# Kernel tuning notes

Measured on AMD Instinct MI355X. Metric: run time of the kernel, lower is better.

## Reference

```python
import jax, jax.numpy as jnp
import numpy as np

WH, WW = 12, 12          # window height/width
N = WH * WW              # tokens per window (144)
HEADS = 16
DIM = 1024
C = DIM // 2             # attention channel dim (512)
HEAD_DIM = C // HEADS    # 32


def _rel_pos_index(wh, ww):
    ch, cw = np.arange(wh), np.arange(ww)
    coords = np.stack(np.meshgrid(ch, cw, indexing='ij')).reshape(2, -1)  # [2, N]
    rel = (coords[:, :, None] - coords[:, None, :]).transpose(1, 2, 0)    # [N, N, 2]
    rel = rel.copy()
    rel[:, :, 0] += wh - 1
    rel[:, :, 1] += ww - 1
    rel[:, :, 0] *= 2 * ww - 1
    return rel.sum(-1)  # [N, N] int


def _layernorm(x, g, b, eps=1e-5):
    mu = jnp.mean(x, axis=-1, keepdims=True)
    var = jnp.mean(jnp.square(x - mu), axis=-1, keepdims=True)
    return (x - mu) * jax.lax.rsqrt(var + eps) * g + b


def setup_inputs():
    key = jax.random.key(0)
    ks = jax.random.split(key, 10)
    std = 0.02
    inp = {
        'x': jax.random.normal(ks[0], (256, N, DIM), jnp.float32),
        'template': jax.random.normal(ks[1], (64, N, DIM), jnp.float32),
        'mask0': jnp.zeros((16, N, N), jnp.float32),
        'mask1': jnp.zeros((4, N, N), jnp.float32),
        's_H': 48, 's_W': 48, 't_H': 24, 't_W': 24,
        'rpb_table': jax.random.normal(ks[2], ((2 * WH - 1) * (2 * WW - 1), HEADS), jnp.float32) * std,
        'w_ps': jax.random.normal(ks[3], (DIM, C), jnp.float32) * std,
        'b_ps': jnp.zeros((C,), jnp.float32),
        'g_ps': jnp.ones((C,), jnp.float32),
        'be_ps': jnp.zeros((C,), jnp.float32),
        'w_pt': jax.random.normal(ks[4], (DIM, C), jnp.float32) * std,
        'b_pt': jnp.zeros((C,), jnp.float32),
        'g_pt': jnp.ones((C,), jnp.float32),
        'be_pt': jnp.zeros((C,), jnp.float32),
        'w_qkv': jax.random.normal(ks[5], (C, 3 * C), jnp.float32) * std,
        'b_qkv': jnp.zeros((3 * C,), jnp.float32),
        'w_tr': jax.random.normal(ks[6], (C, DIM), jnp.float32) * std,
        'b_tr': jnp.zeros((DIM,), jnp.float32),
        'w_sr': jax.random.normal(ks[7], (C, DIM), jnp.float32) * std,
        'b_sr': jnp.zeros((DIM,), jnp.float32),
    }
    return inp


def reference(x, template, mask0, mask1, s_H, s_W, t_H, t_W,
              rpb_table, w_ps, b_ps, g_ps, be_ps, w_pt, b_pt, g_pt, be_pt,
              w_qkv, b_qkv, w_tr, b_tr, w_sr, b_sr):
    scale = HEAD_DIM ** (-0.5)
    search_attn = _layernorm(x @ w_ps + b_ps, g_ps, be_ps)          # [Sw, N, C]
    template_attn = _layernorm(template @ w_pt + b_pt, g_pt, be_pt)  # [Tw, N, C]
    Sw, Tw = search_attn.shape[0], template_attn.shape[0]
    xa = jnp.concatenate([template_attn, search_attn], axis=0)      # [B_, N, C]
    B_, n, c = xa.shape

    qkv = (xa @ w_qkv + b_qkv).reshape(B_, n, 3, HEADS, HEAD_DIM)
    q = qkv[:, :, 0].transpose(0, 2, 1, 3) * scale  # [B_, H, N, Dh]
    k = qkv[:, :, 1].transpose(0, 2, 1, 3)
    v = qkv[:, :, 2].transpose(0, 2, 1, 3)

    idx = _rel_pos_index(WH, WW)  # numpy constant [N, N]
    bias = rpb_table[idx.reshape(-1)].reshape(n, n, HEADS).transpose(2, 0, 1)  # [H, N, N]

    attn = jnp.einsum('bhnd,bhmd->bhnm', q, k) + bias[None]  # [B_, H, N, N]

    attn_t, attn_s = attn[:Tw], attn[Tw:]
    nWs = mask0.shape[0]
    attn_s = (attn_s.reshape(Sw // nWs, nWs, HEADS, n, n) + mask0[None, :, None]).reshape(Sw, HEADS, n, n)
    nWt = mask1.shape[0]
    attn_t = (attn_t.reshape(Tw // nWt, nWt, HEADS, n, n) + mask1[None, :, None]).reshape(Tw, HEADS, n, n)
    attn = jax.nn.softmax(jnp.concatenate([attn_t, attn_s], axis=0), axis=-1)

    out = jnp.einsum('bhnm,bhmd->bhnd', attn, v).transpose(0, 2, 1, 3).reshape(B_, n, c)
    template_out = out[:Tw] @ w_tr + b_tr  # [Tw, N, DIM]
    search_out = out[Tw:] @ w_sr + b_sr    # [Sw, N, DIM]
    return (template_out, search_out)
```

## Files before the change

### kernel.cpp

```cpp
#include <hip/hip_runtime.h>


using s16x8 = __attribute__((ext_vector_type(8))) short;
using f32x4 = __attribute__((ext_vector_type(4))) float;
typedef __attribute__((ext_vector_type(2))) unsigned u32x2;

#define NTOK 144
#define NHEADS 16
#define CDIM 512
#define TROWS 9216
#define SROWS 36864
#define TOTROWS 46080
#define NWIN 320
#define NCLS 20

__device__ __forceinline__ unsigned short f2bf(float f) {
  unsigned u = __float_as_uint(f);
  u += 0x7fffu + ((u >> 16) & 1u);
  return (unsigned short)(u >> 16);
}
__device__ __forceinline__ float bf2f(unsigned short u) {
  return __uint_as_float(((unsigned)u) << 16);
}
__device__ __forceinline__ s16x8 mk8(unsigned a, unsigned b, unsigned c, unsigned d) {
  union { unsigned u[4]; s16x8 v; } x;
  x.u[0] = a; x.u[1] = b; x.u[2] = c; x.u[3] = d;
  return x.v;
}

__device__ __forceinline__ void gld16(const unsigned short* g, short* l) {
  __builtin_amdgcn_global_load_lds(
      (const __attribute__((address_space(1))) unsigned int*)g,
      (__attribute__((address_space(3))) unsigned int*)l, 16, 0, 0);
}


__global__ void transpose_cast(const float* __restrict__ w,
                               unsigned short* __restrict__ wT, int Kd, int Nd,
                               int nScale, float s) {
  int i = blockIdx.x * 256 + threadIdx.x;
  if (i >= Kd * Nd) return;
  int n = i / Kd, k = i % Kd;
  float v = w[(size_t)k * Nd + n];
  if (n < nScale) v *= s;
  wT[i] = f2bf(v);
}

__global__ void scale_bias(const float* __restrict__ in, float* __restrict__ out) {
  int i = blockIdx.x * 256 + threadIdx.x;
  if (i >= 1536) return;
  out[i] = in[i] * (i < 512 ? 0.17677669529663687f : 1.0f);
}

__global__ __launch_bounds__(256) void cast_bf16(const float* __restrict__ in,
                                                 unsigned short* __restrict__ out, int n8) {
  int i = blockIdx.x * 256 + threadIdx.x;
  if (i >= n8) return;
  const float4* p = (const float4*)in + (size_t)i * 2;
  float4 f0 = p[0], f1 = p[1];
  s16x8 o;
  o[0] = (short)f2bf(f0.x); o[1] = (short)f2bf(f0.y);
  o[2] = (short)f2bf(f0.z); o[3] = (short)f2bf(f0.w);
  o[4] = (short)f2bf(f1.x); o[5] = (short)f2bf(f1.y);
  o[6] = (short)f2bf(f1.z); o[7] = (short)f2bf(f1.w);
  *(s16x8*)&out[(size_t)i * 8] = o;
}

__global__ void build_cmb(const float* __restrict__ rpb, const float* __restrict__ m0,
                          const float* __restrict__ m1, unsigned short* __restrict__ cmb) {
  int i = blockIdx.x * 256 + threadIdx.x;
  if (i >= NCLS * NHEADS * NTOK * NTOK) return;
  int cls = i / (NHEADS * NTOK * NTOK);
  int rem = i % (NHEADS * NTOK * NTOK);
  int h = rem / (NTOK * NTOK);
  int ij = rem % (NTOK * NTOK);
  int qi = ij / NTOK, kj = ij % NTOK;
  int dh = qi / 12 - kj / 12 + 11;
  int dw = qi % 12 - kj % 12 + 11;
  float bias = rpb[(dh * 23 + dw) * NHEADS + h];
  float mv = (cls < 4) ? m1[(size_t)cls * NTOK * NTOK + ij]
                       : m0[(size_t)(cls - 4) * NTOK * NTOK + ij];
  cmb[i] = f2bf(bias + mv);
}

template<int EPI>
__global__ __launch_bounds__(256) void gemm_glds(
    const unsigned short* __restrict__ Ab,
    const unsigned short* __restrict__ BTt, const unsigned short* __restrict__ BTs,
    const float* __restrict__ biast, const float* __restrict__ biass,
    void* __restrict__ Cout, int M, int N, int K)
{
  __shared__ short As[2][128 * 64];
  __shared__ short Bs[2][128 * 64];
  const int t = threadIdx.x;
  const int lane = t & 63, wv = t >> 6, lg = lane >> 4, lc = lane & 15;

  const int id = blockIdx.x + gridDim.x * blockIdx.y;
  const int chunk = (gridDim.x * gridDim.y) >> 3;
  const int lid = (id & 7) * chunk + (id >> 3);
  const int bn = (lid % gridDim.x) * 128, bm = (lid / gridDim.x) * 128;

  const bool isT = bm < TROWS;
  const unsigned short* BT = isT ? BTt : BTs;
  const float* bias = isT ? biast : biass;

  const int srow = 32 * wv + (lane >> 3);
  const int scol = ((lane & 7) ^ ((lane >> 3) & 7)) * 8;
  const unsigned short* aSrc = Ab + (size_t)(bm + srow) * K + scol;
  const unsigned short* bSrc = BT + (size_t)(bn + srow) * K + scol;
  const size_t rowK8 = (size_t)8 * K;

  f32x4 acc[2][8] = {};

  auto STAGE = [&](int b, int kt) {
#pragma unroll
    for (int i = 0; i < 4; i++) {
      gld16(aSrc + kt + i * rowK8, &As[b][(wv * 4 + i) * 512]);
      gld16(bSrc + kt + i * rowK8, &Bs[b][(wv * 4 + i) * 512]);
    }
  };
  auto COMPUTE = [&](int b) {
#pragma unroll
    for (int kk = 0; kk < 2; kk++) {
      const int csw = 8 * ((4 * kk + lg) ^ (lc & 7));
      const int r0 = wv * 32 + lc, r1 = r0 + 16;
      s16x8 a0 = *(const s16x8*)&As[b][r0 * 64 + csw];
      s16x8 a1 = *(const s16x8*)&As[b][r1 * 64 + csw];
#pragma unroll
      for (int nt = 0; nt < 8; nt++) {
        s16x8 bfr = *(const s16x8*)&Bs[b][(nt * 16 + lc) * 64 + csw];
        acc[0][nt] = __builtin_amdgcn_mfma_f32_16x16x32_bf16(a0, bfr, acc[0][nt], 0, 0, 0);
        acc[1][nt] = __builtin_amdgcn_mfma_f32_16x16x32_bf16(a1, bfr, acc[1][nt], 0, 0, 0);
      }
    }
  };

  STAGE(0, 0);
  __syncthreads();
  int cur = 0;
  for (int kt = 64; kt < K; kt += 64) {
    STAGE(cur ^ 1, kt);
    COMPUTE(cur);
    __syncthreads();
    cur ^= 1;
  }
  COMPUTE(cur);

#pragma unroll
  for (int mt = 0; mt < 2; mt++) {
    const int rbase = bm + wv * 32 + mt * 16 + lg * 4;
#pragma unroll
    for (int nt = 0; nt < 8; nt++) {
      const int cg = bn + nt * 16 + lc;
#pragma unroll
      for (int r = 0; r < 4; r++) {
        const int rg = rbase + r;
        float val = acc[mt][nt][r] + bias[cg];
        if (EPI == 2) {
          ((float*)Cout)[(size_t)rg * N + cg] = val;
        } else {
          ((unsigned short*)Cout)[(size_t)rg * N + cg] = f2bf(val);
        }
      }
    }
  }
}

__global__ __launch_bounds__(256) void ln_kernel(
    unsigned short* __restrict__ xa,
    const float* __restrict__ g_pt, const float* __restrict__ be_pt,
    const float* __restrict__ g_ps, const float* __restrict__ be_ps)
{
  const int row = blockIdx.x * 4 + (threadIdx.x >> 6);
  const int lane = threadIdx.x & 63;
  const bool isT = row < TROWS;
  const float* gg = isT ? g_pt : g_ps;
  const float* be = isT ? be_pt : be_ps;
  unsigned short* p = xa + (size_t)row * CDIM;
  const int c0 = lane * 8;

  s16x8 v8 = *(const s16x8*)&p[c0];
  float f[8];
  float s = 0.f, s2 = 0.f;
#pragma unroll
  for (int i = 0; i < 8; i++) {
    float xv = bf2f((unsigned short)v8[i]);
    f[i] = xv; s += xv; s2 += xv * xv;
  }
#pragma unroll
  for (int d = 1; d < 64; d <<= 1) { s += __shfl_xor(s, d); s2 += __shfl_xor(s2, d); }
  float mu = s * (1.f / CDIM);
  float var = s2 * (1.f / CDIM) - mu * mu;
  float rs = rsqrtf(var + 1e-5f);

  float4 g0 = *(const float4*)&gg[c0], g1 = *(const float4*)&gg[c0 + 4];
  float4 e0 = *(const float4*)&be[c0], e1 = *(const float4*)&be[c0 + 4];
  float gv[8] = {g0.x, g0.y, g0.z, g0.w, g1.x, g1.y, g1.z, g1.w};
  float ev[8] = {e0.x, e0.y, e0.z, e0.w, e1.x, e1.y, e1.z, e1.w};
  s16x8 o;
#pragma unroll
  for (int i = 0; i < 8; i++)
    o[i] = (short)f2bf((f[i] - mu) * rs * gv[i] + ev[i]);
  *(s16x8*)&p[c0] = o;
}

__global__ __launch_bounds__(576) void attn_kernel(
    const unsigned short* __restrict__ qkv, const unsigned short* __restrict__ cmb,
    unsigned short* __restrict__ outp)
{
  __shared__ short VT[32 * 168];
  const int nb = NWIN * NHEADS;
  const int lid = (blockIdx.x & 7) * (nb >> 3) + (blockIdx.x >> 3);
  const int w = lid >> 4, h = lid & 15;
  const int t = threadIdx.x;
  const unsigned short* qb = qkv + (size_t)w * NTOK * 1536;
  const int hq = h * 32;

  {
    const int n = t >> 2, d0 = (t & 3) * 8;
    s16x8 vv = *(const s16x8*)&qb[(size_t)n * 1536 + 1024 + hq + d0];
#pragma unroll
    for (int i = 0; i < 8; i++) VT[(d0 + i) * 168 + n] = vv[i];
  }
  if (t < 512) VT[(t >> 4) * 168 + 144 + (t & 15)] = 0;

  const int lane = t & 63, wv = t >> 6, lg = lane >> 4, lc = lane & 15;
  const int q = wv * 16 + lc;
  const f32x4 zero = {0.f, 0.f, 0.f, 0.f};

  const s16x8 qf = *(const s16x8*)&qb[(size_t)q * 1536 + hq + lg * 8];

  const int cls = (w < 64) ? (w & 3) : 4 + ((w - 64) & 15);
  const unsigned short* cm =
      cmb + ((size_t)cls * NHEADS + h) * (NTOK * NTOK) + (size_t)q * NTOK;
  uint2 cmr[9];
#pragma unroll
  for (int nt = 0; nt < 9; nt++)
    cmr[nt] = *(const uint2*)&cm[nt * 16 + lg * 4];

  f32x4 accS[9];
#pragma unroll
  for (int nt = 0; nt < 9; nt++) {
    s16x8 kf = *(const s16x8*)&qb[(size_t)(nt * 16 + lc) * 1536 + 512 + hq + lg * 8];
    accS[nt] = __builtin_amdgcn_mfma_f32_16x16x32_bf16(kf, qf, zero, 0, 0, 0);
  }

  float mx = -1e30f;
#pragma unroll
  for (int nt = 0; nt < 9; nt++) {
    accS[nt][0] += bf2f((unsigned short)(cmr[nt].x & 0xffff));
    accS[nt][1] += bf2f((unsigned short)(cmr[nt].x >> 16));
    accS[nt][2] += bf2f((unsigned short)(cmr[nt].y & 0xffff));
    accS[nt][3] += bf2f((unsigned short)(cmr[nt].y >> 16));
#pragma unroll
    for (int r = 0; r < 4; r++) mx = fmaxf(mx, accS[nt][r]);
  }
  mx = fmaxf(mx, __shfl_xor(mx, 16));
  mx = fmaxf(mx, __shfl_xor(mx, 32));

  float sum = 0.f;
#pragma unroll
  for (int nt = 0; nt < 9; nt++)
#pragma unroll
    for (int r = 0; r < 4; r++) {
      float e = __expf(accS[nt][r] - mx);
      accS[nt][r] = e;
      sum += e;
    }
  sum += __shfl_xor(sum, 16);
  sum += __shfl_xor(sum, 32);
  const float inv = 1.f / sum;

  unsigned pk0[9], pk1[9];
#pragma unroll
  for (int nt = 0; nt < 9; nt++) {
    pk0[nt] = (unsigned)f2bf(accS[nt][0]) | ((unsigned)f2bf(accS[nt][1]) << 16);
    pk1[nt] = (unsigned)f2bf(accS[nt][2]) | ((unsigned)f2bf(accS[nt][3]) << 16);
  }

  __syncthreads();

#pragma unroll
  for (int dt = 0; dt < 2; dt++) {
    const short* vbase = &VT[(dt * 16 + lc) * 168];
    f32x4 accO = zero;
#pragma unroll
    for (int kk = 0; kk < 4; kk++) {
      u32x2 A0 = *(const u32x2*)&vbase[32 * kk + lg * 4];
      u32x2 A1 = *(const u32x2*)&vbase[32 * kk + 16 + lg * 4];
      s16x8 a = mk8(A0[0], A0[1], A1[0], A1[1]);
      s16x8 b = mk8(pk0[2 * kk], pk1[2 * kk], pk0[2 * kk + 1], pk1[2 * kk + 1]);
      accO = __builtin_amdgcn_mfma_f32_16x16x32_bf16(a, b, accO, 0, 0, 0);
    }
    {
      u32x2 A0 = *(const u32x2*)&vbase[128 + lg * 4];
      s16x8 a = mk8(A0[0], A0[1], 0u, 0u);
      s16x8 b = mk8(pk0[8], pk1[8], 0u, 0u);
      accO = __builtin_amdgcn_mfma_f32_16x16x32_bf16(a, b, accO, 0, 0, 0);
    }
    unsigned o0 = (unsigned)f2bf(accO[0] * inv) | ((unsigned)f2bf(accO[1] * inv) << 16);
    unsigned o1 = (unsigned)f2bf(accO[2] * inv) | ((unsigned)f2bf(accO[3] * inv) << 16);
    uint2 st; st.x = o0; st.y = o1;
    *(uint2*)&outp[(size_t)(w * NTOK + q) * CDIM + hq + dt * 16 + lg * 4] = st;
  }
}

extern "C" void kernel_launch(void* const* d_in, const int* in_sizes, int n_in,
                              void* d_out, int out_size, void* d_ws, size_t ws_size,
                              hipStream_t stream)
{
  const float* x     = (const float*)d_in[0];
  const float* tpl   = (const float*)d_in[1];
  const float* mask0 = (const float*)d_in[2];
  const float* mask1 = (const float*)d_in[3];
  const float* rpb   = (const float*)d_in[8];
  const float* w_ps  = (const float*)d_in[9];
  const float* b_ps  = (const float*)d_in[10];
  const float* g_ps  = (const float*)d_in[11];
  const float* be_ps = (const float*)d_in[12];
  const float* w_pt  = (const float*)d_in[13];
  const float* b_pt  = (const float*)d_in[14];
  const float* g_pt  = (const float*)d_in[15];
  const float* be_pt = (const float*)d_in[16];
  const float* w_qkv = (const float*)d_in[17];
  const float* b_qkv = (const float*)d_in[18];
  const float* w_tr  = (const float*)d_in[19];
  const float* b_tr  = (const float*)d_in[20];
  const float* w_sr  = (const float*)d_in[21];
  const float* b_sr  = (const float*)d_in[22];

  char* ws = (char*)d_ws;
  unsigned short* wpsT  = (unsigned short*)(ws + 0x0000000);
  unsigned short* wptT  = (unsigned short*)(ws + 0x0100000);
  unsigned short* wqkvT = (unsigned short*)(ws + 0x0200000);
  unsigned short* wtrT  = (unsigned short*)(ws + 0x0380000);
  unsigned short* wsrT  = (unsigned short*)(ws + 0x0480000);
  unsigned short* cmb   = (unsigned short*)(ws + 0x0580000);
  float* bqS            = (float*)(ws + 0x12F0000);
  unsigned short* xa    = (unsigned short*)(ws + 0x1300000);
  unsigned short* Sa    = (unsigned short*)(ws + 0x4000000);
  unsigned short* qkvF  = (unsigned short*)(ws + 0x4000000);
  float* outb           = (float*)d_out;

  transpose_cast<<<2048, 256, 0, stream>>>(w_ps, wpsT, 1024, 512, 0, 1.f);
  transpose_cast<<<2048, 256, 0, stream>>>(w_pt, wptT, 1024, 512, 0, 1.f);
  transpose_cast<<<3072, 256, 0, stream>>>(w_qkv, wqkvT, 512, 1536,
                                           512, 0.17677669529663687f);
  transpose_cast<<<2048, 256, 0, stream>>>(w_tr, wtrT, 512, 1024, 0, 1.f);
  transpose_cast<<<2048, 256, 0, stream>>>(w_sr, wsrT, 512, 1024, 0, 1.f);
  scale_bias<<<6, 256, 0, stream>>>(b_qkv, bqS);
  build_cmb<<<(NCLS * NHEADS * NTOK * NTOK + 255) / 256, 256, 0, stream>>>(rpb, mask0, mask1, cmb);

  cast_bf16<<<(TROWS * 1024 / 8 + 255) / 256, 256, 0, stream>>>(tpl, Sa, TROWS * 1024 / 8);
  cast_bf16<<<(SROWS * 1024 / 8 + 255) / 256, 256, 0, stream>>>(
      x, Sa + (size_t)TROWS * 1024, SROWS * 1024 / 8);

  gemm_glds<0><<<dim3(4, 360), 256, 0, stream>>>(Sa, wptT, wpsT, b_pt, b_ps,
                                                 xa, TOTROWS, CDIM, 1024);
  ln_kernel<<<TOTROWS / 4, 256, 0, stream>>>(xa, g_pt, be_pt, g_ps, be_ps);

  gemm_glds<0><<<dim3(12, 360), 256, 0, stream>>>(xa, wqkvT, wqkvT, bqS, bqS,
                                                  qkvF, TOTROWS, 1536, CDIM);
  attn_kernel<<<NWIN * NHEADS, 576, 0, stream>>>(qkvF, cmb, xa);

  gemm_glds<2><<<dim3(8, 360), 256, 0, stream>>>(xa, wtrT, wsrT, b_tr, b_sr,
                                                 outb, TOTROWS, 1024, CDIM);
}
```

Measured before the change: 472.6 us.

## Fuse fp32-to-bf16 input cast into projection GEMM and relax pipeline barriers

Drops the separate cast_bf16 passes over x and template. A new GEMM streams fp32 activations straight into LDS and converts them to bf16 in registers with v_cvt_pk_bf16_f32 just before the MFMA, which saves writing and re-reading a bf16 copy of the inputs. The GEMM main loops also swap __syncthreads for explicit vmcnt waits plus s_barrier so the next tile's loads overlap compute. In exchange the fused kernel uses 64-row tiles with twice the LDS for A and converts A again for every N tile, so the fp32 input is read four times.

Result: faster. 461.9 us (-2.3%).

```diff
diff --git a/kernel.cpp b/kernel.cpp
--- a/kernel.cpp
+++ b/kernel.cpp
@@ -27,8 +27,13 @@
   x.u[0] = a; x.u[1] = b; x.u[2] = c; x.u[3] = d;
   return x.v;
 }
-
-__device__ __forceinline__ void gld16(const unsigned short* g, short* l) {
+__device__ __forceinline__ unsigned pkbf(float a, float b) {
+  unsigned r;
+  asm("v_cvt_pk_bf16_f32 %0, %1, %2" : "=v"(r) : "v"(a), "v"(b));
+  return r;
+}
+
+__device__ __forceinline__ void gld16(const void* g, void* l) {
   __builtin_amdgcn_global_load_lds(
       (const __attribute__((address_space(1))) unsigned int*)g,
       (__attribute__((address_space(3))) unsigned int*)l, 16, 0, 0);
@@ -50,20 +55,6 @@
   int i = blockIdx.x * 256 + threadIdx.x;
   if (i >= 1536) return;
   out[i] = in[i] * (i < 512 ? 0.17677669529663687f : 1.0f);
-}
-
-__global__ __launch_bounds__(256) void cast_bf16(const float* __restrict__ in,
-                                                 unsigned short* __restrict__ out, int n8) {
-  int i = blockIdx.x * 256 + threadIdx.x;
-  if (i >= n8) return;
-  const float4* p = (const float4*)in + (size_t)i * 2;
-  float4 f0 = p[0], f1 = p[1];
-  s16x8 o;
-  o[0] = (short)f2bf(f0.x); o[1] = (short)f2bf(f0.y);
-  o[2] = (short)f2bf(f0.z); o[3] = (short)f2bf(f0.w);
-  o[4] = (short)f2bf(f1.x); o[5] = (short)f2bf(f1.y);
-  o[6] = (short)f2bf(f1.z); o[7] = (short)f2bf(f1.w);
-  *(s16x8*)&out[(size_t)i * 8] = o;
 }
 
 __global__ void build_cmb(const float* __restrict__ rpb, const float* __restrict__ m0,
@@ -136,14 +127,19 @@
   };
 
   STAGE(0, 0);
-  __syncthreads();
   int cur = 0;
   for (int kt = 64; kt < K; kt += 64) {
     STAGE(cur ^ 1, kt);
+    asm volatile("s_waitcnt vmcnt(8)" ::: "memory");
+    __builtin_amdgcn_s_barrier();
+    __builtin_amdgcn_sched_barrier(0);
     COMPUTE(cur);
-    __syncthreads();
+    __builtin_amdgcn_s_barrier();
     cur ^= 1;
   }
+  asm volatile("s_waitcnt vmcnt(0)" ::: "memory");
+  __builtin_amdgcn_s_barrier();
+  __builtin_amdgcn_sched_barrier(0);
   COMPUTE(cur);
 
 #pragma unroll
@@ -156,13 +152,93 @@
       for (int r = 0; r < 4; r++) {
         const int rg = rbase + r;
         float val = acc[mt][nt][r] + bias[cg];
-        if (EPI == 2) {
-          ((float*)Cout)[(size_t)rg * N + cg] = val;
-        } else {
-          ((unsigned short*)Cout)[(size_t)rg * N + cg] = f2bf(val);
-        }
+        if (EPI == 2) ((float*)Cout)[(size_t)rg * N + cg] = val;
+        else ((unsigned short*)Cout)[(size_t)rg * N + cg] = f2bf(val);
       }
     }
+  }
+}
+
+__global__ __launch_bounds__(256) void gemm_f32a(
+    const float* __restrict__ At, const float* __restrict__ Asrch,
+    const unsigned short* __restrict__ BTt, const unsigned short* __restrict__ BTs,
+    const float* __restrict__ biast, const float* __restrict__ biass,
+    unsigned short* __restrict__ Cout, int M, int N, int K)
+{
+  __shared__ float Asf[2][64 * 64];
+  __shared__ short Bs[2][128 * 64];
+  const int t = threadIdx.x;
+  const int lane = t & 63, wv = t >> 6, lg = lane >> 4, lc = lane & 15;
+
+  const int id = blockIdx.x + gridDim.x * blockIdx.y;
+  const int chunk = (gridDim.x * gridDim.y) >> 3;
+  const int lid = (id & 7) * chunk + (id >> 3);
+  const int bn = (lid % gridDim.x) * 128, bm = (lid / gridDim.x) * 64;
+
+  const bool isT = bm < TROWS;
+  const float* Af = isT ? At : (Asrch - (size_t)TROWS * K);
+  const unsigned short* BT = isT ? BTt : BTs;
+  const float* bias = isT ? biast : biass;
+
+  const int arow = wv * 16 + (lane >> 4);
+  const int brow = 32 * wv + (lane >> 3);
+  const int bcol = ((lane & 7) ^ ((lane >> 3) & 7)) * 8;
+  const unsigned short* bSrc = BT + (size_t)(bn + brow) * K + bcol;
+  const size_t rowK8 = (size_t)8 * K;
+
+  f32x4 acc[8] = {};
+
+  auto STAGE = [&](int b, int kt) {
+#pragma unroll
+    for (int i = 0; i < 4; i++) {
+      const int r = arow + i * 4;
+      const int sg = ((lane & 15) ^ (r & 15)) * 4;
+      gld16(Af + (size_t)(bm + r) * K + kt + sg, &Asf[b][(wv * 16 + i * 4) * 64]);
+      gld16(bSrc + kt + i * rowK8, &Bs[b][(wv * 4 + i) * 512]);
+    }
+  };
+  auto COMPUTE = [&](int b) {
+#pragma unroll
+    for (int kk = 0; kk < 2; kk++) {
+      const int G0 = 2 * (4 * kk + lg);
+      const int r0 = wv * 16 + lc;
+      const float* arowp = &Asf[b][r0 * 64];
+      float4 x0 = *(const float4*)&arowp[(G0 ^ lc) * 4];
+      float4 x1 = *(const float4*)&arowp[((G0 + 1) ^ lc) * 4];
+      s16x8 a0 = mk8(pkbf(x0.x, x0.y), pkbf(x0.z, x0.w),
+                     pkbf(x1.x, x1.y), pkbf(x1.z, x1.w));
+      const int csw = 8 * ((4 * kk + lg) ^ (lc & 7));
+#pragma unroll
+      for (int nt = 0; nt < 8; nt++) {
+        s16x8 bfr = *(const s16x8*)&Bs[b][(nt * 16 + lc) * 64 + csw];
+        acc[nt] = __builtin_amdgcn_mfma_f32_16x16x32_bf16(a0, bfr, acc[nt], 0, 0, 0);
+      }
+    }
+  };
+
+  STAGE(0, 0);
+  int cur = 0;
+  for (int kt = 64; kt < K; kt += 64) {
+    STAGE(cur ^ 1, kt);
+    asm volatile("s_waitcnt vmcnt(8)" ::: "memory");
+    __builtin_amdgcn_s_barrier();
+    __builtin_amdgcn_sched_barrier(0);
+    COMPUTE(cur);
+    __builtin_amdgcn_s_barrier();
+    cur ^= 1;
+  }
+  asm volatile("s_waitcnt vmcnt(0)" ::: "memory");
+  __builtin_amdgcn_s_barrier();
+  __builtin_amdgcn_sched_barrier(0);
+  COMPUTE(cur);
+
+  const int rbase = bm + wv * 16 + lg * 4;
+#pragma unroll
+  for (int nt = 0; nt < 8; nt++) {
+    const int cg = bn + nt * 16 + lc;
+#pragma unroll
+    for (int r = 0; r < 4; r++)
+      Cout[(size_t)(rbase + r) * N + cg] = f2bf(acc[nt][r] + bias[cg]);
   }
 }
 
@@ -338,7 +414,6 @@
   unsigned short* cmb   = (unsigned short*)(ws + 0x0580000);
   float* bqS            = (float*)(ws + 0x12F0000);
   unsigned short* xa    = (unsigned short*)(ws + 0x1300000);
-  unsigned short* Sa    = (unsigned short*)(ws + 0x4000000);
   unsigned short* qkvF  = (unsigned short*)(ws + 0x4000000);
   float* outb           = (float*)d_out;
 
@@ -351,12 +426,8 @@
   scale_bias<<<6, 256, 0, stream>>>(b_qkv, bqS);
   build_cmb<<<(NCLS * NHEADS * NTOK * NTOK + 255) / 256, 256, 0, stream>>>(rpb, mask0, mask1, cmb);
 
-  cast_bf16<<<(TROWS * 1024 / 8 + 255) / 256, 256, 0, stream>>>(tpl, Sa, TROWS * 1024 / 8);
-  cast_bf16<<<(SROWS * 1024 / 8 + 255) / 256, 256, 0, stream>>>(
-      x, Sa + (size_t)TROWS * 1024, SROWS * 1024 / 8);
-
-  gemm_glds<0><<<dim3(4, 360), 256, 0, stream>>>(Sa, wptT, wpsT, b_pt, b_ps,
-                                                 xa, TOTROWS, CDIM, 1024);
+  gemm_f32a<<<dim3(4, 720), 256, 0, stream>>>(tpl, x, wptT, wpsT, b_pt, b_ps,
+                                              xa, TOTROWS, CDIM, 1024);
   ln_kernel<<<TOTROWS / 4, 256, 0, stream>>>(xa, g_pt, be_pt, g_ps, be_ps);
 
   gemm_glds<0><<<dim3(12, 360), 256, 0, stream>>>(xa, wqkvT, wqkvT, bqS, bqS,
```
